# Performance work log

Measured on AMD Instinct MI355X. Metric: run time of the kernel, lower is better.

The kernel has to match this reference:

```python
import jax, jax.numpy as jnp
import numpy as np

H = 64          # HIDDEN_DIM
V = 64          # VOCAB_SIZE
THR = 0.4       # ENERGY_THRESHOLD
LN_EPS = 1e-5
NORM_EPS = 1e-12


def _layer_norm(x, g, b):
    mu = jnp.mean(x, axis=-1, keepdims=True)
    var = jnp.var(x, axis=-1, keepdims=True)
    return (x - mu) * jax.lax.rsqrt(var + LN_EPS) * g + b


def setup_inputs() -> dict:
    key = jax.random.key(0)
    ks = jax.random.split(key, 12)
    B, L = 256, 2048
    s = 0.05
    return {
        "x": jax.random.randint(ks[0], (B, L), 0, V),
        "embed": jax.random.normal(ks[1], (V, H), jnp.float32) * s,
        "w1": jax.random.normal(ks[2], (H, 2 * H), jnp.float32) * s,
        "b1": jnp.zeros((2 * H,), jnp.float32),
        "w2": jax.random.normal(ks[3], (2 * H, H), jnp.float32) * s,
        "b2": jnp.zeros((H,), jnp.float32),
        "ln_g": jnp.ones((H,), jnp.float32),
        "ln_b": jnp.zeros((H,), jnp.float32),
        "wk": jax.random.normal(ks[4], (H, H), jnp.float32) * s,
        "wv": jax.random.normal(ks[5], (H, H), jnp.float32) * s,
        "wq": jax.random.normal(ks[6], (H, H), jnp.float32) * s,
        "wo": jax.random.normal(ks[7], (H, V), jnp.float32) * s,
        "bo": jnp.zeros((V,), jnp.float32),
    }


def reference(x, embed, w1, b1, w2, b2, ln_g, ln_b, wk, wv, wq, wo, bo):
    # Encoder: embed -> FFN -> residual -> LayerNorm
    h = embed[x]                                        # [B, L, H]
    ff = jax.nn.relu(h @ w1 + b1) @ w2 + b2
    h = _layer_norm(h + ff, ln_g, ln_b)                 # [B, L, H]

    B = h.shape[0]
    # Precompute all k (L2-normalized) and v projections, then scan over time.
    k = h @ wk                                          # [B, L, H]
    k = k / jnp.maximum(jnp.linalg.norm(k, axis=-1, keepdims=True), NORM_EPS)
    v = h @ wv                                          # [B, L, H]

    def step(M, kv):
        k_t, v_t = kv                                   # each [B, H]
        pred = jnp.einsum('bij,bj->bi', M, k_t)         # [B, H]
        delta = v_t - pred
        gate = (jnp.linalg.norm(delta, axis=-1, keepdims=True)
                > THR * jnp.linalg.norm(v_t, axis=-1, keepdims=True)).astype(M.dtype)
        M = M + gate[:, :, None] * jnp.einsum('bi,bj->bij', delta, k_t)
        return M, None

    M0 = jnp.zeros((B, H, H), h.dtype)
    M, _ = jax.lax.scan(step, M0,
                        (jnp.swapaxes(k, 0, 1), jnp.swapaxes(v, 0, 1)))

    q = h[:, -1, :] @ wq                                # [B, H]
    read = jax.nn.relu(jnp.einsum('bij,bj->bi', M, q))  # [B, H]
    return read @ wo + bo                               # [B, V]
```

## Files before the change

kernel.cpp:

```cpp
#include <hip/hip_runtime.h>
#include <hip/hip_bf16.h>

#define HD   64
#define SEQ  2048
#define NB   256
#define TWOH 128
#define NCH  32

typedef float v4f __attribute__((ext_vector_type(4)));

template <int CTRL>
__device__ __forceinline__ float dpp_add(float x) {
    int y = __builtin_amdgcn_update_dpp(0, __builtin_bit_cast(int, x),
                                        CTRL, 0xF, 0xF, true);
    return x + __builtin_bit_cast(float, y);
}

__device__ __forceinline__ float wave_total(float x) {
    x = dpp_add<0x111>(x);
    x = dpp_add<0x112>(x);
    x = dpp_add<0x114>(x);
    x = dpp_add<0x118>(x);
    x = dpp_add<0x142>(x);
    x = dpp_add<0x143>(x);
    return __builtin_bit_cast(float,
        __builtin_amdgcn_readlane(__builtin_bit_cast(int, x), 63));
}

__device__ __forceinline__ float bcastf(float v, int l) {
    return __builtin_bit_cast(float,
        __builtin_amdgcn_readlane(__builtin_bit_cast(int, v), l));
}

__device__ __forceinline__ float hsum4(v4f a) {
    return (a.x + a.y) + (a.z + a.w);
}

__device__ __forceinline__ bool detect_bf16(const void* embed, int lane) {
    const unsigned short* u = (const unsigned short*)embed;
    int bad = 0;
    for (int i = 2 * lane; i < 4096; i += 128) {
        float v = __uint_as_float(((unsigned int)u[i]) << 16);
        if (!(fabsf(v) < 1e4f)) bad = 1;
    }
    return !__any(bad);
}

template <bool BF>
__device__ __forceinline__ float ldf(const void* p, int i) {
    if (BF) return __bfloat162float(((const __hip_bfloat16*)p)[i]);
    return ((const float*)p)[i];
}

#define LGKM_BARRIER() asm volatile("s_waitcnt lgkmcnt(0)" ::: "memory")

template <bool BF>
__device__ void encode_stream(int wid, int lane, int tl, const void* embed,
                              const void* w1, const void* b1, const void* w2,
                              const void* b2, const void* ln_g, const void* ln_b,
                              const void* wk, const void* wvp, const void* wq,
                              float* __restrict__ k_lds, float* __restrict__ v_lds,
                              float* __restrict__ thr2_lds,
                              float* __restrict__ qrow,
                              float* __restrict__ hb,
                              float* __restrict__ ub) {
    const int tbase = wid * 16;
    float h[16];
    #pragma unroll
    for (int it = 0; it < 16; ++it) {
        h[it] = ldf<BF>(embed, (tbase + it) * HD + lane);
        hb[it * HD + lane] = h[it];
    }
    LGKM_BARRIER();

    float u0[16], u1[16];
    #pragma unroll
    for (int it = 0; it < 16; ++it) { u0[it] = 0.f; u1[it] = 0.f; }
    #pragma unroll 1
    for (int j4 = 0; j4 < 16; ++j4) {
        const int j = j4 * 4;
        float wa0 = ldf<BF>(w1, (j + 0) * TWOH + lane);
        float wb0 = ldf<BF>(w1, (j + 0) * TWOH + lane + HD);
        float wa1 = ldf<BF>(w1, (j + 1) * TWOH + lane);
        float wb1 = ldf<BF>(w1, (j + 1) * TWOH + lane + HD);
        float wa2 = ldf<BF>(w1, (j + 2) * TWOH + lane);
        float wb2 = ldf<BF>(w1, (j + 2) * TWOH + lane + HD);
        float wa3 = ldf<BF>(w1, (j + 3) * TWOH + lane);
        float wb3 = ldf<BF>(w1, (j + 3) * TWOH + lane + HD);
        #pragma unroll
        for (int it = 0; it < 16; ++it) {
            const v4f hj = *(const v4f*)&hb[it * HD + j];
            u0[it] = fmaf(hj.x, wa0, u0[it]); u1[it] = fmaf(hj.x, wb0, u1[it]);
            u0[it] = fmaf(hj.y, wa1, u0[it]); u1[it] = fmaf(hj.y, wb1, u1[it]);
            u0[it] = fmaf(hj.z, wa2, u0[it]); u1[it] = fmaf(hj.z, wb2, u1[it]);
            u0[it] = fmaf(hj.w, wa3, u0[it]); u1[it] = fmaf(hj.w, wb3, u1[it]);
        }
    }
    const float bb0 = ldf<BF>(b1, lane), bb1 = ldf<BF>(b1, lane + HD);
    #pragma unroll
    for (int it = 0; it < 16; ++it) {
        u0[it] = fmaxf(u0[it] + bb0, 0.f);
        u1[it] = fmaxf(u1[it] + bb1, 0.f);
    }

    float f[16];
    #pragma unroll
    for (int it = 0; it < 16; ++it) f[it] = 0.f;
    LGKM_BARRIER();
    #pragma unroll
    for (int it = 0; it < 16; ++it) ub[it * HD + lane] = u0[it];
    LGKM_BARRIER();
    #pragma unroll 1
    for (int e4 = 0; e4 < 16; ++e4) {
        const int e = e4 * 4;
        float w0 = ldf<BF>(w2, (e + 0) * HD + lane);
        float w1v = ldf<BF>(w2, (e + 1) * HD + lane);
        float w2v = ldf<BF>(w2, (e + 2) * HD + lane);
        float w3 = ldf<BF>(w2, (e + 3) * HD + lane);
        #pragma unroll
        for (int it = 0; it < 16; ++it) {
            const v4f ue = *(const v4f*)&ub[it * HD + e];
            f[it] = fmaf(ue.x, w0, f[it]);
            f[it] = fmaf(ue.y, w1v, f[it]);
            f[it] = fmaf(ue.z, w2v, f[it]);
            f[it] = fmaf(ue.w, w3, f[it]);
        }
    }
    LGKM_BARRIER();
    #pragma unroll
    for (int it = 0; it < 16; ++it) ub[it * HD + lane] = u1[it];
    LGKM_BARRIER();
    #pragma unroll 1
    for (int e4 = 0; e4 < 16; ++e4) {
        const int e = e4 * 4;
        float w0 = ldf<BF>(w2, (HD + e + 0) * HD + lane);
        float w1v = ldf<BF>(w2, (HD + e + 1) * HD + lane);
        float w2v = ldf<BF>(w2, (HD + e + 2) * HD + lane);
        float w3 = ldf<BF>(w2, (HD + e + 3) * HD + lane);
        #pragma unroll
        for (int it = 0; it < 16; ++it) {
            const v4f ue = *(const v4f*)&ub[it * HD + e];
            f[it] = fmaf(ue.x, w0, f[it]);
            f[it] = fmaf(ue.y, w1v, f[it]);
            f[it] = fmaf(ue.z, w2v, f[it]);
            f[it] = fmaf(ue.w, w3, f[it]);
        }
    }
    const float b2v = ldf<BF>(b2, lane);
    const float lg = ldf<BF>(ln_g, lane), lb = ldf<BF>(ln_b, lane);

    LGKM_BARRIER();
    #pragma unroll 1
    for (int it = 0; it < 16; ++it) {
        float y = h[it] + f[it] + b2v;
        float mu  = wave_total(y) * 0.015625f;
        float dvv = y - mu;
        float var = wave_total(dvv * dvv) * 0.015625f;
        float hn  = fmaf(dvv * (1.f / sqrtf(var + 1e-5f)), lg, lb);
        hb[it * HD + lane] = hn;
    }
    LGKM_BARRIER();

    float k[16], v[16];
    #pragma unroll
    for (int it = 0; it < 16; ++it) { k[it] = 0.f; v[it] = 0.f; }
    #pragma unroll 1
    for (int j4 = 0; j4 < 16; ++j4) {
        const int j = j4 * 4;
        float ka = ldf<BF>(wk, (j + 0) * HD + lane);
        float kb = ldf<BF>(wk, (j + 1) * HD + lane);
        float kc = ldf<BF>(wk, (j + 2) * HD + lane);
        float kd = ldf<BF>(wk, (j + 3) * HD + lane);
        float va = ldf<BF>(wvp, (j + 0) * HD + lane);
        float vb = ldf<BF>(wvp, (j + 1) * HD + lane);
        float vc = ldf<BF>(wvp, (j + 2) * HD + lane);
        float vd = ldf<BF>(wvp, (j + 3) * HD + lane);
        #pragma unroll
        for (int it = 0; it < 16; ++it) {
            const v4f hj = *(const v4f*)&hb[it * HD + j];
            k[it] = fmaf(hj.x, ka, k[it]); v[it] = fmaf(hj.x, va, v[it]);
            k[it] = fmaf(hj.y, kb, k[it]); v[it] = fmaf(hj.y, vb, v[it]);
            k[it] = fmaf(hj.z, kc, k[it]); v[it] = fmaf(hj.z, vc, v[it]);
            k[it] = fmaf(hj.w, kd, k[it]); v[it] = fmaf(hj.w, vd, v[it]);
        }
    }
    #pragma unroll 1
    for (int it = 0; it < 16; ++it) {
        const int t = tbase + it;
        float nk = sqrtf(wave_total(k[it] * k[it]));
        float kn = k[it] / fmaxf(nk, 1e-12f);
        float nv2 = wave_total(v[it] * v[it]);
        k_lds[t * HD + lane] = kn;
        v_lds[t * HD + lane] = v[it];
        if (lane == 0) thr2_lds[t] = 0.16f * nv2;
    }
    if (tl >= tbase && tl < tbase + 16) {
        float q = 0.f;
        const int it = tl - tbase;
        #pragma unroll
        for (int j4 = 0; j4 < 16; ++j4) {
            const v4f hj = *(const v4f*)&hb[it * HD + j4 * 4];
            q = fmaf(hj.x, ldf<BF>(wq, (j4 * 4 + 0) * HD + lane), q);
            q = fmaf(hj.y, ldf<BF>(wq, (j4 * 4 + 1) * HD + lane), q);
            q = fmaf(hj.z, ldf<BF>(wq, (j4 * 4 + 2) * HD + lane), q);
            q = fmaf(hj.w, ldf<BF>(wq, (j4 * 4 + 3) * HD + lane), q);
        }
        qrow[lane] = q;
    }
}

__global__ __launch_bounds__(256, 1) void fused_kernel(
    const int* __restrict__ x, const void* embed, const void* w1,
    const void* b1, const void* w2, const void* b2, const void* ln_g,
    const void* ln_b, const void* wk, const void* wvp, const void* wq,
    const void* wo, const void* bo, void* __restrict__ out) {
    const int b = blockIdx.x, tid = threadIdx.x;
    const int wid = tid >> 6, lane = tid & 63;
    __shared__ __align__(16) float k_lds[4096];
    __shared__ __align__(16) float v_lds[4096];
    __shared__ __align__(16) float gu_lds[4096];
    __shared__ __align__(16) float hbuf[4096];
    __shared__ int   tok_lds[SEQ];
    __shared__ float thr2_lds[64];
    __shared__ float qrow[64];
    __shared__ float pbuf[2][4][64];
    __shared__ __align__(16) float rd_lds[64];

    const int* xr = x + b * SEQ;
    #pragma unroll
    for (int c = 0; c < 8; ++c) tok_lds[c * 256 + tid] = xr[c * 256 + tid];
    const int tl = xr[SEQ - 1];

    const bool bf = detect_bf16(embed, lane);
    if (bf)
        encode_stream<true>(wid, lane, tl, embed, w1, b1, w2, b2, ln_g, ln_b,
                            wk, wvp, wq, k_lds, v_lds, thr2_lds, qrow,
                            &hbuf[wid * 1024], &gu_lds[wid * 1024]);
    else
        encode_stream<false>(wid, lane, tl, embed, w1, b1, w2, b2, ln_g, ln_b,
                             wk, wvp, wq, k_lds, v_lds, thr2_lds, qrow,
                             &hbuf[wid * 1024], &gu_lds[wid * 1024]);
    __syncthreads();

    const float thr2 = thr2_lds[lane];

    v4f kreg[16];
    #pragma unroll
    for (int i = 0; i < 16; ++i)
        kreg[i] = *(const v4f*)&k_lds[lane * HD + i * 4];

    v4f cacc = {0.f, 0.f, 0.f, 0.f};
    #pragma unroll
    for (int i = 0; i < 16; ++i) {
        const v4f qv = *(const v4f*)&qrow[i * 4];
        cacc = __builtin_elementwise_fma(qv, kreg[i], cacc);
    }
    const float cq = hsum4(cacc);

    #pragma unroll 1
    for (int t0 = 0; t0 < 16; ++t0) {
        const int t = wid * 16 + t0;
        const float* kt = &k_lds[t * HD];
        v4f a = {0.f, 0.f, 0.f, 0.f};
        #pragma unroll
        for (int i = 0; i < 16; ++i) {
            const v4f kv = *(const v4f*)&kt[i * 4];
            a = __builtin_elementwise_fma(kv, kreg[i], a);
        }
        gu_lds[t * HD + lane] = hsum4(a);
    }

    v4f dv[4], R[4];
    v4f acc = {0.f, 0.f, 0.f, 0.f};
    #pragma unroll
    for (int i = 0; i < 4; ++i) {
        dv[i] = *(const v4f*)&v_lds[lane * HD + wid * 16 + i * 4];
        R[i]  = (v4f){0.f, 0.f, 0.f, 0.f};
        acc   = __builtin_elementwise_fma(dv[i], dv[i], acc);
    }
    pbuf[0][wid][lane] = hsum4(acc);
    int pp = 1;
    __syncthreads();
    float nd2 = ((pbuf[0][0][lane] + pbuf[0][1][lane]) +
                 (pbuf[0][2][lane] + pbuf[0][3][lane]));
    unsigned long long fireset = __ballot(nd2 > thr2);

    int chunk = tok_lds[lane];
    #pragma unroll 1
    for (int c = 0; c < NCH; ++c) {
        int nxt = 0;
        if (c + 1 < NCH) nxt = tok_lds[(c + 1) * 64 + lane];
        unsigned long long pend = __ballot((int)((fireset >> chunk) & 1ull));
        while (pend) {
            const int s = __builtin_ctzll(pend);
            const int t = __builtin_amdgcn_readlane(chunk, s);
            const float g   = gu_lds[t * HD + lane];
            const float cqt = bcastf(cq, t);
            const v4f gs  = {-g, -g, -g, -g};
            const v4f cqs = {cqt, cqt, cqt, cqt};
            v4f q4 = {0.f, 0.f, 0.f, 0.f};
            #pragma unroll
            for (int i = 0; i < 4; ++i) {
                v4f sve;
                sve.x = bcastf(dv[i].x, t);
                sve.y = bcastf(dv[i].y, t);
                sve.z = bcastf(dv[i].z, t);
                sve.w = bcastf(dv[i].w, t);
                dv[i] = __builtin_elementwise_fma(gs, sve, dv[i]);
                R[i]  = __builtin_elementwise_fma(cqs, sve, R[i]);
                q4    = __builtin_elementwise_fma(dv[i], dv[i], q4);
            }
            pbuf[pp][wid][lane] = hsum4(q4);
            __syncthreads();
            nd2 = ((pbuf[pp][0][lane] + pbuf[pp][1][lane]) +
                   (pbuf[pp][2][lane] + pbuf[pp][3][lane]));
            pp ^= 1;
            fireset = __ballot(nd2 > thr2);
            const unsigned long long above =
                (s >= 63) ? 0ull : (~0ull << (s + 1));
            pend = __ballot((int)((fireset >> chunk) & 1ull)) & above;
        }
        chunk = nxt;
    }

    if (lane == 0) {
        #pragma unroll
        for (int i = 0; i < 4; ++i) {
            v4f r = R[i];
            r.x = fmaxf(r.x, 0.f); r.y = fmaxf(r.y, 0.f);
            r.z = fmaxf(r.z, 0.f); r.w = fmaxf(r.w, 0.f);
            *(v4f*)&rd_lds[wid * 16 + i * 4] = r;
        }
    }
    __syncthreads();

    if (wid == 0) {
        if (bf) {
            float acc2 = __bfloat162float(((const __hip_bfloat16*)bo)[lane]);
            #pragma unroll 8
            for (int j = 0; j < HD; ++j)
                acc2 = fmaf(rd_lds[j],
                    __bfloat162float(((const __hip_bfloat16*)wo)[j * HD + lane]),
                    acc2);
            ((__hip_bfloat16*)out)[b * HD + lane] = __float2bfloat16(acc2);
        } else {
            float acc2 = ((const float*)bo)[lane];
            #pragma unroll 8
            for (int j = 0; j < HD; ++j)
                acc2 = fmaf(rd_lds[j], ((const float*)wo)[j * HD + lane], acc2);
            ((float*)out)[b * HD + lane] = acc2;
        }
    }
}

extern "C" void kernel_launch(void* const* d_in, const int* in_sizes, int n_in,
                              void* d_out, int out_size, void* d_ws, size_t ws_size,
                              hipStream_t stream) {
    const int* x      = (const int*)d_in[0];
    const void* embed = d_in[1];
    const void* w1    = d_in[2];
    const void* b1    = d_in[3];
    const void* w2    = d_in[4];
    const void* b2    = d_in[5];
    const void* ln_g  = d_in[6];
    const void* ln_b  = d_in[7];
    const void* wk    = d_in[8];
    const void* wvp   = d_in[9];
    const void* wq    = d_in[10];
    const void* wo    = d_in[11];
    const void* bo    = d_in[12];

    fused_kernel<<<NB, 256, 0, stream>>>(x, embed, w1, b1, w2, b2, ln_g, ln_b,
                                         wk, wvp, wq, wo, bo, d_out);
}
```

Baseline: 283.5 us.

## Stage encoder weights in LDS and software-prefetch weight rows

All 256 threads cooperatively copy w1, w2, wk and wv into shared memory once per block, and the encoder matmul loops then read weights from LDS instead of issuing per-wave global loads. Each loop also loads the next iteration's weight row ahead of the FMA block. The h/u scratch buffers are aliased onto k_lds/v_lds, and the gram buffer reuses w1_lds to keep LDS within budget. The q projection is moved before the k/v write-out. This adds an upfront copy plus a block barrier and raises LDS use, in exchange for cutting global-load latency in the encoder.

```diff
diff --git a/kernel.cpp b/kernel.cpp
--- a/kernel.cpp
+++ b/kernel.cpp
@@ -55,16 +55,33 @@
 #define LGKM_BARRIER() asm volatile("s_waitcnt lgkmcnt(0)" ::: "memory")
 
 template <bool BF>
-__device__ void encode_stream(int wid, int lane, int tl, const void* embed,
-                              const void* w1, const void* b1, const void* w2,
-                              const void* b2, const void* ln_g, const void* ln_b,
-                              const void* wk, const void* wvp, const void* wq,
-                              float* __restrict__ k_lds, float* __restrict__ v_lds,
-                              float* __restrict__ thr2_lds,
-                              float* __restrict__ qrow,
-                              float* __restrict__ hb,
-                              float* __restrict__ ub) {
+__device__ void stage_and_encode(int tid, int wid, int lane, int tl,
+                                 const void* embed, const void* w1,
+                                 const void* b1, const void* w2, const void* b2,
+                                 const void* ln_g, const void* ln_b,
+                                 const void* wk, const void* wvp, const void* wq,
+                                 float* __restrict__ w1_lds,
+                                 float* __restrict__ w2_lds,
+                                 float* __restrict__ wk_lds,
+                                 float* __restrict__ wv_lds,
+                                 float* __restrict__ k_lds,
+                                 float* __restrict__ v_lds,
+                                 float* __restrict__ thr2_lds,
+                                 float* __restrict__ qrow_s) {
+    #pragma unroll 8
+    for (int i = tid; i < 8192; i += 256) w1_lds[i] = ldf<BF>(w1, i);
+    #pragma unroll 8
+    for (int i = tid; i < 8192; i += 256) w2_lds[i] = ldf<BF>(w2, i);
+    #pragma unroll 8
+    for (int i = tid; i < 4096; i += 256) wk_lds[i] = ldf<BF>(wk, i);
+    #pragma unroll 8
+    for (int i = tid; i < 4096; i += 256) wv_lds[i] = ldf<BF>(wvp, i);
+    __syncthreads();
+
     const int tbase = wid * 16;
+    float* hb = &k_lds[wid * 1024];
+    float* ub = &v_lds[wid * 1024];
+
     float h[16];
     #pragma unroll
     for (int it = 0; it < 16; ++it) {
@@ -76,25 +93,36 @@
     float u0[16], u1[16];
     #pragma unroll
     for (int it = 0; it < 16; ++it) { u0[it] = 0.f; u1[it] = 0.f; }
+    float a0 = w1_lds[0 * TWOH + lane], b0 = w1_lds[0 * TWOH + lane + HD];
+    float a1 = w1_lds[1 * TWOH + lane], b1w = w1_lds[1 * TWOH + lane + HD];
+    float a2 = w1_lds[2 * TWOH + lane], b2w = w1_lds[2 * TWOH + lane + HD];
+    float a3 = w1_lds[3 * TWOH + lane], b3w = w1_lds[3 * TWOH + lane + HD];
     #pragma unroll 1
     for (int j4 = 0; j4 < 16; ++j4) {
+        float na0 = 0, nb0 = 0, na1 = 0, nb1 = 0,
+              na2 = 0, nb2 = 0, na3 = 0, nb3 = 0;
+        if (j4 < 15) {
+            const int j = (j4 + 1) * 4;
+            na0 = w1_lds[(j + 0) * TWOH + lane];
+            nb0 = w1_lds[(j + 0) * TWOH + lane + HD];
+            na1 = w1_lds[(j + 1) * TWOH + lane];
+            nb1 = w1_lds[(j + 1) * TWOH + lane + HD];
+            na2 = w1_lds[(j + 2) * TWOH + lane];
+            nb2 = w1_lds[(j + 2) * TWOH + lane + HD];
+            na3 = w1_lds[(j + 3) * TWOH + lane];
+            nb3 = w1_lds[(j + 3) * TWOH + lane + HD];
+        }
         const int j = j4 * 4;
-        float wa0 = ldf<BF>(w1, (j + 0) * TWOH + lane);
-        float wb0 = ldf<BF>(w1, (j + 0) * TWOH + lane + HD);
-        float wa1 = ldf<BF>(w1, (j + 1) * TWOH + lane);
-        float wb1 = ldf<BF>(w1, (j + 1) * TWOH + lane + HD);
-        float wa2 = ldf<BF>(w1, (j + 2) * TWOH + lane);
-        float wb2 = ldf<BF>(w1, (j + 2) * TWOH + lane + HD);
-        float wa3 = ldf<BF>(w1, (j + 3) * TWOH + lane);
-        float wb3 = ldf<BF>(w1, (j + 3) * TWOH + lane + HD);
         #pragma unroll
         for (int it = 0; it < 16; ++it) {
             const v4f hj = *(const v4f*)&hb[it * HD + j];
-            u0[it] = fmaf(hj.x, wa0, u0[it]); u1[it] = fmaf(hj.x, wb0, u1[it]);
-            u0[it] = fmaf(hj.y, wa1, u0[it]); u1[it] = fmaf(hj.y, wb1, u1[it]);
-            u0[it] = fmaf(hj.z, wa2, u0[it]); u1[it] = fmaf(hj.z, wb2, u1[it]);
-            u0[it] = fmaf(hj.w, wa3, u0[it]); u1[it] = fmaf(hj.w, wb3, u1[it]);
-        }
+            u0[it] = fmaf(hj.x, a0, u0[it]); u1[it] = fmaf(hj.x, b0, u1[it]);
+            u0[it] = fmaf(hj.y, a1, u0[it]); u1[it] = fmaf(hj.y, b1w, u1[it]);
+            u0[it] = fmaf(hj.z, a2, u0[it]); u1[it] = fmaf(hj.z, b2w, u1[it]);
+            u0[it] = fmaf(hj.w, a3, u0[it]); u1[it] = fmaf(hj.w, b3w, u1[it]);
+        }
+        a0 = na0; b0 = nb0; a1 = na1; b1w = nb1;
+        a2 = na2; b2w = nb2; a3 = na3; b3w = nb3;
     }
     const float bb0 = ldf<BF>(b1, lane), bb1 = ldf<BF>(b1, lane + HD);
     #pragma unroll
@@ -106,44 +134,42 @@
     float f[16];
     #pragma unroll
     for (int it = 0; it < 16; ++it) f[it] = 0.f;
-    LGKM_BARRIER();
     #pragma unroll
     for (int it = 0; it < 16; ++it) ub[it * HD + lane] = u0[it];
     LGKM_BARRIER();
     #pragma unroll 1
-    for (int e4 = 0; e4 < 16; ++e4) {
-        const int e = e4 * 4;
-        float w0 = ldf<BF>(w2, (e + 0) * HD + lane);
-        float w1v = ldf<BF>(w2, (e + 1) * HD + lane);
-        float w2v = ldf<BF>(w2, (e + 2) * HD + lane);
-        float w3 = ldf<BF>(w2, (e + 3) * HD + lane);
-        #pragma unroll
-        for (int it = 0; it < 16; ++it) {
-            const v4f ue = *(const v4f*)&ub[it * HD + e];
-            f[it] = fmaf(ue.x, w0, f[it]);
-            f[it] = fmaf(ue.y, w1v, f[it]);
-            f[it] = fmaf(ue.z, w2v, f[it]);
-            f[it] = fmaf(ue.w, w3, f[it]);
-        }
-    }
-    LGKM_BARRIER();
-    #pragma unroll
-    for (int it = 0; it < 16; ++it) ub[it * HD + lane] = u1[it];
-    LGKM_BARRIER();
-    #pragma unroll 1
-    for (int e4 = 0; e4 < 16; ++e4) {
-        const int e = e4 * 4;
-        float w0 = ldf<BF>(w2, (HD + e + 0) * HD + lane);
-        float w1v = ldf<BF>(w2, (HD + e + 1) * HD + lane);
-        float w2v = ldf<BF>(w2, (HD + e + 2) * HD + lane);
-        float w3 = ldf<BF>(w2, (HD + e + 3) * HD + lane);
-        #pragma unroll
-        for (int it = 0; it < 16; ++it) {
-            const v4f ue = *(const v4f*)&ub[it * HD + e];
-            f[it] = fmaf(ue.x, w0, f[it]);
-            f[it] = fmaf(ue.y, w1v, f[it]);
-            f[it] = fmaf(ue.z, w2v, f[it]);
-            f[it] = fmaf(ue.w, w3, f[it]);
+    for (int pass = 0; pass < 2; ++pass) {
+        const int ebase = pass * HD;
+        float w0 = w2_lds[(ebase + 0) * HD + lane];
+        float w1v = w2_lds[(ebase + 1) * HD + lane];
+        float w2v = w2_lds[(ebase + 2) * HD + lane];
+        float w3 = w2_lds[(ebase + 3) * HD + lane];
+        #pragma unroll 1
+        for (int e4 = 0; e4 < 16; ++e4) {
+            float n0 = 0, n1 = 0, n2 = 0, n3 = 0;
+            if (e4 < 15) {
+                const int e = ebase + (e4 + 1) * 4;
+                n0 = w2_lds[(e + 0) * HD + lane];
+                n1 = w2_lds[(e + 1) * HD + lane];
+                n2 = w2_lds[(e + 2) * HD + lane];
+                n3 = w2_lds[(e + 3) * HD + lane];
+            }
+            const int e = e4 * 4;
+            #pragma unroll
+            for (int it = 0; it < 16; ++it) {
+                const v4f ue = *(const v4f*)&ub[it * HD + e];
+                f[it] = fmaf(ue.x, w0, f[it]);
+                f[it] = fmaf(ue.y, w1v, f[it]);
+                f[it] = fmaf(ue.z, w2v, f[it]);
+                f[it] = fmaf(ue.w, w3, f[it]);
+            }
+            w0 = n0; w1v = n1; w2v = n2; w3 = n3;
+        }
+        if (pass == 0) {
+            LGKM_BARRIER();
+            #pragma unroll
+            for (int it = 0; it < 16; ++it) ub[it * HD + lane] = u1[it];
+            LGKM_BARRIER();
         }
     }
     const float b2v = ldf<BF>(b2, lane);
@@ -164,17 +190,26 @@
     float k[16], v[16];
     #pragma unroll
     for (int it = 0; it < 16; ++it) { k[it] = 0.f; v[it] = 0.f; }
+    float ka = wk_lds[0 * HD + lane], kb = wk_lds[1 * HD + lane];
+    float kc = wk_lds[2 * HD + lane], kd = wk_lds[3 * HD + lane];
+    float va = wv_lds[0 * HD + lane], vb = wv_lds[1 * HD + lane];
+    float vc = wv_lds[2 * HD + lane], vd = wv_lds[3 * HD + lane];
     #pragma unroll 1
     for (int j4 = 0; j4 < 16; ++j4) {
+        float nka = 0, nkb = 0, nkc = 0, nkd = 0,
+              nva = 0, nvb = 0, nvc = 0, nvd = 0;
+        if (j4 < 15) {
+            const int j = (j4 + 1) * 4;
+            nka = wk_lds[(j + 0) * HD + lane];
+            nkb = wk_lds[(j + 1) * HD + lane];
+            nkc = wk_lds[(j + 2) * HD + lane];
+            nkd = wk_lds[(j + 3) * HD + lane];
+            nva = wv_lds[(j + 0) * HD + lane];
+            nvb = wv_lds[(j + 1) * HD + lane];
+            nvc = wv_lds[(j + 2) * HD + lane];
+            nvd = wv_lds[(j + 3) * HD + lane];
+        }
         const int j = j4 * 4;
-        float ka = ldf<BF>(wk, (j + 0) * HD + lane);
-        float kb = ldf<BF>(wk, (j + 1) * HD + lane);
-        float kc = ldf<BF>(wk, (j + 2) * HD + lane);
-        float kd = ldf<BF>(wk, (j + 3) * HD + lane);
-        float va = ldf<BF>(wvp, (j + 0) * HD + lane);
-        float vb = ldf<BF>(wvp, (j + 1) * HD + lane);
-        float vc = ldf<BF>(wvp, (j + 2) * HD + lane);
-        float vd = ldf<BF>(wvp, (j + 3) * HD + lane);
         #pragma unroll
         for (int it = 0; it < 16; ++it) {
             const v4f hj = *(const v4f*)&hb[it * HD + j];
@@ -183,7 +218,25 @@
             k[it] = fmaf(hj.z, kc, k[it]); v[it] = fmaf(hj.z, vc, v[it]);
             k[it] = fmaf(hj.w, kd, k[it]); v[it] = fmaf(hj.w, vd, v[it]);
         }
-    }
+        ka = nka; kb = nkb; kc = nkc; kd = nkd;
+        va = nva; vb = nvb; vc = nvc; vd = nvd;
+    }
+
+    if (tl >= tbase && tl < tbase + 16) {
+        const int it = tl - tbase;
+        float q = 0.f;
+        #pragma unroll
+        for (int j4 = 0; j4 < 16; ++j4) {
+            const v4f hj = *(const v4f*)&hb[it * HD + j4 * 4];
+            q = fmaf(hj.x, ldf<BF>(wq, (j4 * 4 + 0) * HD + lane), q);
+            q = fmaf(hj.y, ldf<BF>(wq, (j4 * 4 + 1) * HD + lane), q);
+            q = fmaf(hj.z, ldf<BF>(wq, (j4 * 4 + 2) * HD + lane), q);
+            q = fmaf(hj.w, ldf<BF>(wq, (j4 * 4 + 3) * HD + lane), q);
+        }
+        qrow_s[lane] = q;
+    }
+
+    LGKM_BARRIER();
     #pragma unroll 1
     for (int it = 0; it < 16; ++it) {
         const int t = tbase + it;
@@ -194,19 +247,6 @@
         v_lds[t * HD + lane] = v[it];
         if (lane == 0) thr2_lds[t] = 0.16f * nv2;
     }
-    if (tl >= tbase && tl < tbase + 16) {
-        float q = 0.f;
-        const int it = tl - tbase;
-        #pragma unroll
-        for (int j4 = 0; j4 < 16; ++j4) {
-            const v4f hj = *(const v4f*)&hb[it * HD + j4 * 4];
-            q = fmaf(hj.x, ldf<BF>(wq, (j4 * 4 + 0) * HD + lane), q);
-            q = fmaf(hj.y, ldf<BF>(wq, (j4 * 4 + 1) * HD + lane), q);
-            q = fmaf(hj.z, ldf<BF>(wq, (j4 * 4 + 2) * HD + lane), q);
-            q = fmaf(hj.w, ldf<BF>(wq, (j4 * 4 + 3) * HD + lane), q);
-        }
-        qrow[lane] = q;
-    }
 }
 
 __global__ __launch_bounds__(256, 1) void fused_kernel(
@@ -216,13 +256,15 @@
     const void* wo, const void* bo, void* __restrict__ out) {
     const int b = blockIdx.x, tid = threadIdx.x;
     const int wid = tid >> 6, lane = tid & 63;
+    __shared__ __align__(16) float w1_lds[8192];
+    __shared__ __align__(16) float w2_lds[8192];
+    __shared__ __align__(16) float wk_lds[4096];
+    __shared__ __align__(16) float wv_lds[4096];
     __shared__ __align__(16) float k_lds[4096];
     __shared__ __align__(16) float v_lds[4096];
-    __shared__ __align__(16) float gu_lds[4096];
-    __shared__ __align__(16) float hbuf[4096];
     __shared__ int   tok_lds[SEQ];
     __shared__ float thr2_lds[64];
-    __shared__ float qrow[64];
+    __shared__ float qrow_s[64];
     __shared__ float pbuf[2][4][64];
     __shared__ __align__(16) float rd_lds[64];
 
@@ -233,16 +275,17 @@
 
     const bool bf = detect_bf16(embed, lane);
     if (bf)
-        encode_stream<true>(wid, lane, tl, embed, w1, b1, w2, b2, ln_g, ln_b,
-                            wk, wvp, wq, k_lds, v_lds, thr2_lds, qrow,
-                            &hbuf[wid * 1024], &gu_lds[wid * 1024]);
+        stage_and_encode<true>(tid, wid, lane, tl, embed, w1, b1, w2, b2,
+                               ln_g, ln_b, wk, wvp, wq, w1_lds, w2_lds,
+                               wk_lds, wv_lds, k_lds, v_lds, thr2_lds, qrow_s);
     else
-        encode_stream<false>(wid, lane, tl, embed, w1, b1, w2, b2, ln_g, ln_b,
-                             wk, wvp, wq, k_lds, v_lds, thr2_lds, qrow,
-                             &hbuf[wid * 1024], &gu_lds[wid * 1024]);
+        stage_and_encode<false>(tid, wid, lane, tl, embed, w1, b1, w2, b2,
+                                ln_g, ln_b, wk, wvp, wq, w1_lds, w2_lds,
+                                wk_lds, wv_lds, k_lds, v_lds, thr2_lds, qrow_s);
     __syncthreads();
 
     const float thr2 = thr2_lds[lane];
+    float* g_lds = w1_lds;
 
     v4f kreg[16];
     #pragma unroll
@@ -252,7 +295,7 @@
     v4f cacc = {0.f, 0.f, 0.f, 0.f};
     #pragma unroll
     for (int i = 0; i < 16; ++i) {
-        const v4f qv = *(const v4f*)&qrow[i * 4];
+        const v4f qv = *(const v4f*)&qrow_s[i * 4];
         cacc = __builtin_elementwise_fma(qv, kreg[i], cacc);
     }
     const float cq = hsum4(cacc);
@@ -267,7 +310,7 @@
             const v4f kv = *(const v4f*)&kt[i * 4];
             a = __builtin_elementwise_fma(kv, kreg[i], a);
         }
-        gu_lds[t * HD + lane] = hsum4(a);
+        g_lds[t * HD + lane] = hsum4(a);
     }
 
     v4f dv[4], R[4];
@@ -294,7 +337,7 @@
         while (pend) {
             const int s = __builtin_ctzll(pend);
             const int t = __builtin_amdgcn_readlane(chunk, s);
-            const float g   = gu_lds[t * HD + lane];
+            const float g   = g_lds[t * HD + lane];
             const float cqt = bcastf(cq, t);
             const v4f gs  = {-g, -g, -g, -g};
             const v4f cqs = {cqt, cqt, cqt, cqt};
```

New measurement: 306.9 us. 1.08x slower.

## Keep encoder activations in registers with lane broadcasts and pad k/v LDS rows

Applied to the files above, without the earlier changes.

The encoder now keeps h, the FFN hidden activations and the normalized h in registers. It broadcasts individual elements across the wave with bcastf instead of staging them through LDS and reading them back, which removes the hbuf/ub scratch buffers and their waitcnt barriers. Weight rows are software-prefetched one iteration ahead. The k/v LDS rows are padded to a stride of 68 to reduce bank conflicts on the per-lane row reads. The risks are more cross-lane broadcast instructions, since each needs a readlane or ds_bpermute-style op, and higher register pressure from the prefetch registers and the extra arrays.

```diff
diff --git a/kernel.cpp b/kernel.cpp
--- a/kernel.cpp
+++ b/kernel.cpp
@@ -6,6 +6,7 @@
 #define NB   256
 #define TWOH 128
 #define NCH  32
+#define KS   68
 
 typedef float v4f __attribute__((ext_vector_type(4)));
 
@@ -52,49 +53,56 @@
     return ((const float*)p)[i];
 }
 
-#define LGKM_BARRIER() asm volatile("s_waitcnt lgkmcnt(0)" ::: "memory")
-
 template <bool BF>
-__device__ void encode_stream(int wid, int lane, int tl, const void* embed,
-                              const void* w1, const void* b1, const void* w2,
-                              const void* b2, const void* ln_g, const void* ln_b,
-                              const void* wk, const void* wvp, const void* wq,
-                              float* __restrict__ k_lds, float* __restrict__ v_lds,
-                              float* __restrict__ thr2_lds,
-                              float* __restrict__ qrow,
-                              float* __restrict__ hb,
-                              float* __restrict__ ub) {
+__device__ void encode_reg(int wid, int lane, int tl, const void* embed,
+                           const void* w1, const void* b1, const void* w2,
+                           const void* b2, const void* ln_g, const void* ln_b,
+                           const void* wk, const void* wvp, const void* wq,
+                           float* __restrict__ k_lds, float* __restrict__ v_lds,
+                           float* __restrict__ thr2_lds,
+                           float* __restrict__ qrow_s) {
     const int tbase = wid * 16;
     float h[16];
     #pragma unroll
-    for (int it = 0; it < 16; ++it) {
+    for (int it = 0; it < 16; ++it)
         h[it] = ldf<BF>(embed, (tbase + it) * HD + lane);
-        hb[it * HD + lane] = h[it];
-    }
-    LGKM_BARRIER();
 
     float u0[16], u1[16];
     #pragma unroll
     for (int it = 0; it < 16; ++it) { u0[it] = 0.f; u1[it] = 0.f; }
+    float a0 = ldf<BF>(w1, 0 * TWOH + lane), b0 = ldf<BF>(w1, 0 * TWOH + lane + HD);
+    float a1 = ldf<BF>(w1, 1 * TWOH + lane), b1w = ldf<BF>(w1, 1 * TWOH + lane + HD);
+    float a2 = ldf<BF>(w1, 2 * TWOH + lane), b2w = ldf<BF>(w1, 2 * TWOH + lane + HD);
+    float a3 = ldf<BF>(w1, 3 * TWOH + lane), b3w = ldf<BF>(w1, 3 * TWOH + lane + HD);
     #pragma unroll 1
     for (int j4 = 0; j4 < 16; ++j4) {
+        float na0 = 0, nb0 = 0, na1 = 0, nb1 = 0,
+              na2 = 0, nb2 = 0, na3 = 0, nb3 = 0;
+        if (j4 < 15) {
+            const int j = (j4 + 1) * 4;
+            na0 = ldf<BF>(w1, (j + 0) * TWOH + lane);
+            nb0 = ldf<BF>(w1, (j + 0) * TWOH + lane + HD);
+            na1 = ldf<BF>(w1, (j + 1) * TWOH + lane);
+            nb1 = ldf<BF>(w1, (j + 1) * TWOH + lane + HD);
+            na2 = ldf<BF>(w1, (j + 2) * TWOH + lane);
+            nb2 = ldf<BF>(w1, (j + 2) * TWOH + lane + HD);
+            na3 = ldf<BF>(w1, (j + 3) * TWOH + lane);
+            nb3 = ldf<BF>(w1, (j + 3) * TWOH + lane + HD);
+        }
         const int j = j4 * 4;
-        float wa0 = ldf<BF>(w1, (j + 0) * TWOH + lane);
-        float wb0 = ldf<BF>(w1, (j + 0) * TWOH + lane + HD);
-        float wa1 = ldf<BF>(w1, (j + 1) * TWOH + lane);
-        float wb1 = ldf<BF>(w1, (j + 1) * TWOH + lane + HD);
-        float wa2 = ldf<BF>(w1, (j + 2) * TWOH + lane);
-        float wb2 = ldf<BF>(w1, (j + 2) * TWOH + lane + HD);
-        float wa3 = ldf<BF>(w1, (j + 3) * TWOH + lane);
-        float wb3 = ldf<BF>(w1, (j + 3) * TWOH + lane + HD);
         #pragma unroll
         for (int it = 0; it < 16; ++it) {
-            const v4f hj = *(const v4f*)&hb[it * HD + j];
-            u0[it] = fmaf(hj.x, wa0, u0[it]); u1[it] = fmaf(hj.x, wb0, u1[it]);
-            u0[it] = fmaf(hj.y, wa1, u0[it]); u1[it] = fmaf(hj.y, wb1, u1[it]);
-            u0[it] = fmaf(hj.z, wa2, u0[it]); u1[it] = fmaf(hj.z, wb2, u1[it]);
-            u0[it] = fmaf(hj.w, wa3, u0[it]); u1[it] = fmaf(hj.w, wb3, u1[it]);
-        }
+            const float s0 = bcastf(h[it], j + 0);
+            const float s1 = bcastf(h[it], j + 1);
+            const float s2 = bcastf(h[it], j + 2);
+            const float s3 = bcastf(h[it], j + 3);
+            u0[it] = fmaf(s0, a0, u0[it]); u1[it] = fmaf(s0, b0, u1[it]);
+            u0[it] = fmaf(s1, a1, u0[it]); u1[it] = fmaf(s1, b1w, u1[it]);
+            u0[it] = fmaf(s2, a2, u0[it]); u1[it] = fmaf(s2, b2w, u1[it]);
+            u0[it] = fmaf(s3, a3, u0[it]); u1[it] = fmaf(s3, b3w, u1[it]);
+        }
+        a0 = na0; b0 = nb0; a1 = na1; b1w = nb1;
+        a2 = na2; b2w = nb2; a3 = na3; b3w = nb3;
     }
     const float bb0 = ldf<BF>(b1, lane), bb1 = ldf<BF>(b1, lane + HD);
     #pragma unroll
@@ -106,106 +114,128 @@
     float f[16];
     #pragma unroll
     for (int it = 0; it < 16; ++it) f[it] = 0.f;
-    LGKM_BARRIER();
-    #pragma unroll
-    for (int it = 0; it < 16; ++it) ub[it * HD + lane] = u0[it];
-    LGKM_BARRIER();
-    #pragma unroll 1
-    for (int e4 = 0; e4 < 16; ++e4) {
-        const int e = e4 * 4;
-        float w0 = ldf<BF>(w2, (e + 0) * HD + lane);
-        float w1v = ldf<BF>(w2, (e + 1) * HD + lane);
-        float w2v = ldf<BF>(w2, (e + 2) * HD + lane);
-        float w3 = ldf<BF>(w2, (e + 3) * HD + lane);
-        #pragma unroll
-        for (int it = 0; it < 16; ++it) {
-            const v4f ue = *(const v4f*)&ub[it * HD + e];
-            f[it] = fmaf(ue.x, w0, f[it]);
-            f[it] = fmaf(ue.y, w1v, f[it]);
-            f[it] = fmaf(ue.z, w2v, f[it]);
-            f[it] = fmaf(ue.w, w3, f[it]);
-        }
-    }
-    LGKM_BARRIER();
-    #pragma unroll
-    for (int it = 0; it < 16; ++it) ub[it * HD + lane] = u1[it];
-    LGKM_BARRIER();
-    #pragma unroll 1
-    for (int e4 = 0; e4 < 16; ++e4) {
-        const int e = e4 * 4;
-        float w0 = ldf<BF>(w2, (HD + e + 0) * HD + lane);
-        float w1v = ldf<BF>(w2, (HD + e + 1) * HD + lane);
-        float w2v = ldf<BF>(w2, (HD + e + 2) * HD + lane);
-        float w3 = ldf<BF>(w2, (HD + e + 3) * HD + lane);
-        #pragma unroll
-        for (int it = 0; it < 16; ++it) {
-            const v4f ue = *(const v4f*)&ub[it * HD + e];
-            f[it] = fmaf(ue.x, w0, f[it]);
-            f[it] = fmaf(ue.y, w1v, f[it]);
-            f[it] = fmaf(ue.z, w2v, f[it]);
-            f[it] = fmaf(ue.w, w3, f[it]);
-        }
-    }
+    {
+        float w0 = ldf<BF>(w2, 0 * HD + lane), w1v = ldf<BF>(w2, 1 * HD + lane);
+        float w2v = ldf<BF>(w2, 2 * HD + lane), w3 = ldf<BF>(w2, 3 * HD + lane);
+        #pragma unroll 1
+        for (int e4 = 0; e4 < 16; ++e4) {
+            float n0 = 0, n1 = 0, n2 = 0, n3 = 0;
+            if (e4 < 15) {
+                const int e = (e4 + 1) * 4;
+                n0 = ldf<BF>(w2, (e + 0) * HD + lane);
+                n1 = ldf<BF>(w2, (e + 1) * HD + lane);
+                n2 = ldf<BF>(w2, (e + 2) * HD + lane);
+                n3 = ldf<BF>(w2, (e + 3) * HD + lane);
+            }
+            const int e = e4 * 4;
+            #pragma unroll
+            for (int it = 0; it < 16; ++it) {
+                f[it] = fmaf(bcastf(u0[it], e + 0), w0, f[it]);
+                f[it] = fmaf(bcastf(u0[it], e + 1), w1v, f[it]);
+                f[it] = fmaf(bcastf(u0[it], e + 2), w2v, f[it]);
+                f[it] = fmaf(bcastf(u0[it], e + 3), w3, f[it]);
+            }
+            w0 = n0; w1v = n1; w2v = n2; w3 = n3;
+        }
+    }
+    {
+        float w0 = ldf<BF>(w2, 64 * HD + lane), w1v = ldf<BF>(w2, 65 * HD + lane);
+        float w2v = ldf<BF>(w2, 66 * HD + lane), w3 = ldf<BF>(w2, 67 * HD + lane);
+        #pragma unroll 1
+        for (int e4 = 0; e4 < 16; ++e4) {
+            float n0 = 0, n1 = 0, n2 = 0, n3 = 0;
+            if (e4 < 15) {
+                const int e = HD + (e4 + 1) * 4;
+                n0 = ldf<BF>(w2, (e + 0) * HD + lane);
+                n1 = ldf<BF>(w2, (e + 1) * HD + lane);
+                n2 = ldf<BF>(w2, (e + 2) * HD + lane);
+                n3 = ldf<BF>(w2, (e + 3) * HD + lane);
+            }
+            const int e = e4 * 4;
+            #pragma unroll
+            for (int it = 0; it < 16; ++it) {
+                f[it] = fmaf(bcastf(u1[it], e + 0), w0, f[it]);
+                f[it] = fmaf(bcastf(u1[it], e + 1), w1v, f[it]);
+                f[it] = fmaf(bcastf(u1[it], e + 2), w2v, f[it]);
+                f[it] = fmaf(bcastf(u1[it], e + 3), w3, f[it]);
+            }
+            w0 = n0; w1v = n1; w2v = n2; w3 = n3;
+        }
+    }
+
     const float b2v = ldf<BF>(b2, lane);
     const float lg = ldf<BF>(ln_g, lane), lb = ldf<BF>(ln_b, lane);
-
-    LGKM_BARRIER();
+    float hn[16];
     #pragma unroll 1
     for (int it = 0; it < 16; ++it) {
         float y = h[it] + f[it] + b2v;
         float mu  = wave_total(y) * 0.015625f;
         float dvv = y - mu;
         float var = wave_total(dvv * dvv) * 0.015625f;
-        float hn  = fmaf(dvv * (1.f / sqrtf(var + 1e-5f)), lg, lb);
-        hb[it * HD + lane] = hn;
-    }
-    LGKM_BARRIER();
+        hn[it] = fmaf(dvv * (1.f / sqrtf(var + 1e-5f)), lg, lb);
+    }
 
     float k[16], v[16];
     #pragma unroll
     for (int it = 0; it < 16; ++it) { k[it] = 0.f; v[it] = 0.f; }
+    float ka = ldf<BF>(wk, 0 * HD + lane), kb = ldf<BF>(wk, 1 * HD + lane);
+    float kc = ldf<BF>(wk, 2 * HD + lane), kd = ldf<BF>(wk, 3 * HD + lane);
+    float va = ldf<BF>(wvp, 0 * HD + lane), vb = ldf<BF>(wvp, 1 * HD + lane);
+    float vc = ldf<BF>(wvp, 2 * HD + lane), vd = ldf<BF>(wvp, 3 * HD + lane);
     #pragma unroll 1
     for (int j4 = 0; j4 < 16; ++j4) {
+        float nka = 0, nkb = 0, nkc = 0, nkd = 0,
+              nva = 0, nvb = 0, nvc = 0, nvd = 0;
+        if (j4 < 15) {
+            const int j = (j4 + 1) * 4;
+            nka = ldf<BF>(wk, (j + 0) * HD + lane);
+            nkb = ldf<BF>(wk, (j + 1) * HD + lane);
+            nkc = ldf<BF>(wk, (j + 2) * HD + lane);
+            nkd = ldf<BF>(wk, (j + 3) * HD + lane);
+            nva = ldf<BF>(wvp, (j + 0) * HD + lane);
+            nvb = ldf<BF>(wvp, (j + 1) * HD + lane);
+            nvc = ldf<BF>(wvp, (j + 2) * HD + lane);
+            nvd = ldf<BF>(wvp, (j + 3) * HD + lane);
+        }
         const int j = j4 * 4;
-        float ka = ldf<BF>(wk, (j + 0) * HD + lane);
-        float kb = ldf<BF>(wk, (j + 1) * HD + lane);
-        float kc = ldf<BF>(wk, (j + 2) * HD + lane);
-        float kd = ldf<BF>(wk, (j + 3) * HD + lane);
-        float va = ldf<BF>(wvp, (j + 0) * HD + lane);
-        float vb = ldf<BF>(wvp, (j + 1) * HD + lane);
-        float vc = ldf<BF>(wvp, (j + 2) * HD + lane);
-        float vd = ldf<BF>(wvp, (j + 3) * HD + lane);
         #pragma unroll
         for (int it = 0; it < 16; ++it) {
-            const v4f hj = *(const v4f*)&hb[it * HD + j];
-            k[it] = fmaf(hj.x, ka, k[it]); v[it] = fmaf(hj.x, va, v[it]);
-            k[it] = fmaf(hj.y, kb, k[it]); v[it] = fmaf(hj.y, vb, v[it]);
-            k[it] = fmaf(hj.z, kc, k[it]); v[it] = fmaf(hj.z, vc, v[it]);
-            k[it] = fmaf(hj.w, kd, k[it]); v[it] = fmaf(hj.w, vd, v[it]);
-        }
-    }
+            const float s0 = bcastf(hn[it], j + 0);
+            const float s1 = bcastf(hn[it], j + 1);
+            const float s2 = bcastf(hn[it], j + 2);
+            const float s3 = bcastf(hn[it], j + 3);
+            k[it] = fmaf(s0, ka, k[it]); v[it] = fmaf(s0, va, v[it]);
+            k[it] = fmaf(s1, kb, k[it]); v[it] = fmaf(s1, vb, v[it]);
+            k[it] = fmaf(s2, kc, k[it]); v[it] = fmaf(s2, vc, v[it]);
+            k[it] = fmaf(s3, kd, k[it]); v[it] = fmaf(s3, vd, v[it]);
+        }
+        ka = nka; kb = nkb; kc = nkc; kd = nkd;
+        va = nva; vb = nvb; vc = nvc; vd = nvd;
+    }
+
     #pragma unroll 1
     for (int it = 0; it < 16; ++it) {
         const int t = tbase + it;
         float nk = sqrtf(wave_total(k[it] * k[it]));
         float kn = k[it] / fmaxf(nk, 1e-12f);
         float nv2 = wave_total(v[it] * v[it]);
-        k_lds[t * HD + lane] = kn;
-        v_lds[t * HD + lane] = v[it];
+        k_lds[t * KS + lane] = kn;
+        v_lds[t * KS + lane] = v[it];
         if (lane == 0) thr2_lds[t] = 0.16f * nv2;
     }
+
     if (tl >= tbase && tl < tbase + 16) {
+        const int it = tl - tbase;
         float q = 0.f;
-        const int it = tl - tbase;
         #pragma unroll
         for (int j4 = 0; j4 < 16; ++j4) {
-            const v4f hj = *(const v4f*)&hb[it * HD + j4 * 4];
-            q = fmaf(hj.x, ldf<BF>(wq, (j4 * 4 + 0) * HD + lane), q);
-            q = fmaf(hj.y, ldf<BF>(wq, (j4 * 4 + 1) * HD + lane), q);
-            q = fmaf(hj.z, ldf<BF>(wq, (j4 * 4 + 2) * HD + lane), q);
-            q = fmaf(hj.w, ldf<BF>(wq, (j4 * 4 + 3) * HD + lane), q);
-        }
-        qrow[lane] = q;
+            const int j = j4 * 4;
+            q = fmaf(bcastf(hn[it], j + 0), ldf<BF>(wq, (j + 0) * HD + lane), q);
+            q = fmaf(bcastf(hn[it], j + 1), ldf<BF>(wq, (j + 1) * HD + lane), q);
+            q = fmaf(bcastf(hn[it], j + 2), ldf<BF>(wq, (j + 2) * HD + lane), q);
+            q = fmaf(bcastf(hn[it], j + 3), ldf<BF>(wq, (j + 3) * HD + lane), q);
+        }
+        qrow_s[lane] = q;
     }
 }
 
@@ -216,13 +246,12 @@
     const void* wo, const void* bo, void* __restrict__ out) {
     const int b = blockIdx.x, tid = threadIdx.x;
     const int wid = tid >> 6, lane = tid & 63;
-    __shared__ __align__(16) float k_lds[4096];
-    __shared__ __align__(16) float v_lds[4096];
-    __shared__ __align__(16) float gu_lds[4096];
-    __shared__ __align__(16) float hbuf[4096];
+    __shared__ __align__(16) float k_lds[64 * KS];
+    __shared__ __align__(16) float v_lds[64 * KS];
+    __shared__ __align__(16) float g_lds[4096];
     __shared__ int   tok_lds[SEQ];
     __shared__ float thr2_lds[64];
-    __shared__ float qrow[64];
+    __shared__ float qrow_s[64];
     __shared__ float pbuf[2][4][64];
     __shared__ __align__(16) float rd_lds[64];
 
@@ -233,13 +262,11 @@
 
     const bool bf = detect_bf16(embed, lane);
     if (bf)
-        encode_stream<true>(wid, lane, tl, embed, w1, b1, w2, b2, ln_g, ln_b,
-                            wk, wvp, wq, k_lds, v_lds, thr2_lds, qrow,
-                            &hbuf[wid * 1024], &gu_lds[wid * 1024]);
+        encode_reg<true>(wid, lane, tl, embed, w1, b1, w2, b2, ln_g, ln_b,
+                         wk, wvp, wq, k_lds, v_lds, thr2_lds, qrow_s);
     else
-        encode_stream<false>(wid, lane, tl, embed, w1, b1, w2, b2, ln_g, ln_b,
-                             wk, wvp, wq, k_lds, v_lds, thr2_lds, qrow,
-                             &hbuf[wid * 1024], &gu_lds[wid * 1024]);
+        encode_reg<false>(wid, lane, tl, embed, w1, b1, w2, b2, ln_g, ln_b,
+                          wk, wvp, wq, k_lds, v_lds, thr2_lds, qrow_s);
     __syncthreads();
 
     const float thr2 = thr2_lds[lane];
@@ -247,12 +274,12 @@
     v4f kreg[16];
     #pragma unroll
     for (int i = 0; i < 16; ++i)
-        kreg[i] = *(const v4f*)&k_lds[lane * HD + i * 4];
+        kreg[i] = *(const v4f*)&k_lds[lane * KS + i * 4];
 
     v4f cacc = {0.f, 0.f, 0.f, 0.f};
     #pragma unroll
     for (int i = 0; i < 16; ++i) {
-        const v4f qv = *(const v4f*)&qrow[i * 4];
+        const v4f qv = *(const v4f*)&qrow_s[i * 4];
         cacc = __builtin_elementwise_fma(qv, kreg[i], cacc);
     }
     const float cq = hsum4(cacc);
@@ -260,21 +287,21 @@
     #pragma unroll 1
     for (int t0 = 0; t0 < 16; ++t0) {
         const int t = wid * 16 + t0;
-        const float* kt = &k_lds[t * HD];
+        const float* kt = &k_lds[t * KS];
         v4f a = {0.f, 0.f, 0.f, 0.f};
         #pragma unroll
         for (int i = 0; i < 16; ++i) {
             const v4f kv = *(const v4f*)&kt[i * 4];
             a = __builtin_elementwise_fma(kv, kreg[i], a);
         }
-        gu_lds[t * HD + lane] = hsum4(a);
+        g_lds[t * HD + lane] = hsum4(a);
     }
 
     v4f dv[4], R[4];
     v4f acc = {0.f, 0.f, 0.f, 0.f};
     #pragma unroll
     for (int i = 0; i < 4; ++i) {
-        dv[i] = *(const v4f*)&v_lds[lane * HD + wid * 16 + i * 4];
+        dv[i] = *(const v4f*)&v_lds[lane * KS + wid * 16 + i * 4];
         R[i]  = (v4f){0.f, 0.f, 0.f, 0.f};
         acc   = __builtin_elementwise_fma(dv[i], dv[i], acc);
     }
@@ -294,7 +321,7 @@
         while (pend) {
             const int s = __builtin_ctzll(pend);
             const int t = __builtin_amdgcn_readlane(chunk, s);
-            const float g   = gu_lds[t * HD + lane];
+            const float g   = g_lds[t * HD + lane];
             const float cqt = bcastf(cq, t);
             const v4f gs  = {-g, -g, -g, -g};
             const v4f cqs = {cqt, cqt, cqt, cqt};
```

New measurement: 295.5 us. 4.3% more time.
